# Kernel optimization log

Hardware: AMD Instinct MI355X
Metric: run time of the kernel (lower is better)

The kernel has to match this reference:

```python
import jax, jax.numpy as jnp
import numpy as np

WINDOW = 24  # rolling window size
C_IN = 7
D_MODEL = 512
B, S = 32, 4096


def setup_inputs() -> dict:
    key = jax.random.key(0)
    k1, k2, k3, k4 = jax.random.split(key, 4)
    x = jax.random.normal(k1, (B, S, C_IN), dtype=jnp.float32)
    x_mark = jax.random.normal(k2, (B, S, 4), dtype=jnp.float32)
    fan_in = 5 * C_IN * 3  # conv1d fan_in = in_channels * kernel_size
    gain = float(np.sqrt(2.0 / (1.0 + 0.01 ** 2)))  # kaiming, leaky_relu a=0.01
    W_conv = jax.random.normal(k3, (D_MODEL, 5 * C_IN, 3), dtype=jnp.float32) * (gain / np.sqrt(fan_in))
    bound = 1.0 / np.sqrt(fan_in)
    b_conv = jax.random.uniform(k4, (D_MODEL,), dtype=jnp.float32, minval=-bound, maxval=bound)
    return {"x": x, "x_mark": x_mark, "W_conv": W_conv, "b_conv": b_conv}


def _rolling_stats(x, window):
    # x: (B, S, F). Replicate-pad (window-1) at the front, then gather windows.
    Bb, Ss, Ff = x.shape
    padded = jnp.concatenate([jnp.repeat(x[:, :1, :], window - 1, axis=1), x], axis=1)
    idx = jnp.arange(Ss)[:, None] + jnp.arange(window)[None, :]  # (S, W)
    win = padded[:, idx, :]  # (B, S, W, F)
    mean = win.mean(axis=2)
    mx = win.max(axis=2)
    mn = win.min(axis=2)
    # torch.std default: unbiased (ddof=1); tiny eps only guards sqrt-at-0
    var = jnp.sum((win - mean[:, :, None, :]) ** 2, axis=2) / (window - 1)
    std = jnp.sqrt(var + 1e-12)
    return jnp.concatenate([x, mean, mx, mn, std], axis=-1)  # (B, S, 5F)


def reference(x, x_mark, W_conv, b_conv):
    feats = _rolling_stats(x, WINDOW)              # (B, S, 5*C_IN)
    h = jnp.transpose(feats, (0, 2, 1))             # (B, C, S)
    # circular padding of 1 on each side along seq (padding_mode='circular')
    h = jnp.concatenate([h[:, :, -1:], h, h[:, :, :1]], axis=-1)
    y = jax.lax.conv_general_dilated(
        h, W_conv, window_strides=(1,), padding='VALID',
        dimension_numbers=('NCH', 'OIH', 'NCH'))
    y = y + b_conv[None, :, None]
    # dropout is identity in eval mode
    return jnp.transpose(y, (0, 2, 1))              # (B, S, D_MODEL)
```

## Files before the change

### kernel.cpp

```cpp
#include <hip/hip_runtime.h>

#define B_    32
#define S_    4096
#define CIN_  7
#define NF_   35
#define D_    512
#define WIN_  24
#define K3_   105
#define P_    120
#define QN_   66

typedef __attribute__((ext_vector_type(8))) short short8;
typedef __attribute__((ext_vector_type(4))) float float4_;

__device__ __forceinline__ unsigned short f2bf(float f) {
    unsigned int u = __builtin_bit_cast(unsigned int, f);
    u += 0x7FFFu + ((u >> 16) & 1u);
    return (unsigned short)(u >> 16);
}

__global__ __launch_bounds__(256) void pack_w_kernel(
    const float* __restrict__ W, short* __restrict__ Bf)
{
    const int slot = blockIdx.x * 256 + threadIdx.x;
    if (slot >= 32 * 4 * 64) return;
    const int l     = slot & 63;
    const int kstep = (slot >> 6) & 3;
    const int nsub  = slot >> 8;
    const int d  = nsub * 16 + (l & 15);
    const int kb = kstep * 32 + (l >> 4) * 8;

    short8 v;
    #pragma unroll
    for (int j = 0; j < 8; ++j) {
        const int kappa = kb + j;
        v[j] = (kappa < K3_) ? (short)f2bf(W[(size_t)d * K3_ + kappa]) : (short)0;
    }
    *(short8*)(Bf + (size_t)slot * 8) = v;
}

template <bool USE_WS>
__global__ __launch_bounds__(512, 4) void fused_mfma_kernel(
    const float* __restrict__ x, const float* __restrict__ W,
    const short* __restrict__ Bf, const float* __restrict__ bias,
    float* __restrict__ out)
{
    __shared__ short sA[64 * P_];

    const int tid = threadIdx.x;
    const int s0  = blockIdx.x * 64;
    const int b   = blockIdx.y;

    if (tid < QN_ * CIN_) {
        const int q = tid / CIN_;
        const int f = tid - q * CIN_;
        int p = s0 - 1 + q;
        const int sm = p < 0 ? p + S_ : (p >= S_ ? p - S_ : p);
        const float* xb = x + (size_t)b * S_ * CIN_ + f;

        float v[WIN_];
        #pragma unroll
        for (int j = 0; j < WIN_; ++j) {
            int sc = sm - (WIN_ - 1) + j;
            sc = sc < 0 ? 0 : sc;
            v[j] = xb[(size_t)sc * CIN_];
        }
        float sum = 0.f, mx = v[0], mn = v[0];
        #pragma unroll
        for (int j = 0; j < WIN_; ++j) {
            sum += v[j];
            mx = fmaxf(mx, v[j]);
            mn = fminf(mn, v[j]);
        }
        const float mean = sum * (1.0f / WIN_);
        float var = 0.f;
        #pragma unroll
        for (int j = 0; j < WIN_; ++j) {
            const float dv = v[j] - mean;
            var = fmaf(dv, dv, var);
        }
        const float sd = sqrtf(var * (1.0f / (WIN_ - 1)) + 1e-12f);

        const float vals[5] = { v[WIN_ - 1], mean, mx, mn, sd };
        #pragma unroll
        for (int k = 0; k < 3; ++k) {
            const int m = q - k;
            if (m >= 0 && m < 64) {
                #pragma unroll
                for (int g = 0; g < 5; ++g) {
                    const int i = f + g * CIN_;
                    sA[m * P_ + i * 3 + k] = (short)f2bf(vals[g]);
                }
            }
        }
    }
    for (int t = tid; t < 64 * (P_ - K3_); t += 512) {
        const int m = t / (P_ - K3_);
        const int c = K3_ + (t - m * (P_ - K3_));
        sA[m * P_ + c] = 0;
    }
    __syncthreads();

    const int w  = tid >> 6;
    const int l  = tid & 63;
    const int lr = l & 15;
    const int lq = l >> 4;

    float4_ acc[4][4];
    #pragma unroll
    for (int n = 0; n < 4; ++n) {
        const float4_ bv = *(const float4_*)(bias + w * 64 + n * 16 + lq * 4);
        #pragma unroll
        for (int m = 0; m < 4; ++m) acc[m][n] = bv;
    }

    #pragma unroll
    for (int ks = 0; ks < 4; ++ks) {
        short8 ff[4];
        #pragma unroll
        for (int m = 0; m < 4; ++m)
            ff[m] = *(const short8*)&sA[(m * 16 + lr) * P_ + ks * 32 + lq * 8];

        short8 wf[4];
        #pragma unroll
        for (int n = 0; n < 4; ++n) {
            if (USE_WS) {
                const int nsub = w * 4 + n;
                wf[n] = *(const short8*)(Bf + ((size_t)(nsub * 4 + ks) * 64 + l) * 8);
            } else {
                const int d  = w * 64 + n * 16 + lr;
                const int kb = ks * 32 + lq * 8;
                short8 t8;
                #pragma unroll
                for (int j = 0; j < 8; ++j)
                    t8[j] = (kb + j < K3_) ? (short)f2bf(W[(size_t)d * K3_ + kb + j])
                                           : (short)0;
                wf[n] = t8;
            }
        }

        #pragma unroll
        for (int m = 0; m < 4; ++m)
            #pragma unroll
            for (int n = 0; n < 4; ++n)
                acc[m][n] = __builtin_amdgcn_mfma_f32_16x16x32_bf16(
                    wf[n], ff[m], acc[m][n], 0, 0, 0);
    }

    #pragma unroll
    for (int m = 0; m < 4; ++m) {
        float* ob = out + ((size_t)(b * S_ + s0 + m * 16 + lr)) * D_
                        + w * 64 + lq * 4;
        #pragma unroll
        for (int n = 0; n < 4; ++n)
            *(float4_*)(ob + n * 16) = acc[m][n];
    }
}

extern "C" void kernel_launch(void* const* d_in, const int* in_sizes, int n_in,
                              void* d_out, int out_size, void* d_ws, size_t ws_size,
                              hipStream_t stream) {
    const float* x      = (const float*)d_in[0];
    const float* W_conv = (const float*)d_in[2];
    const float* b_conv = (const float*)d_in[3];
    float* out = (float*)d_out;

    const size_t bf_bytes = (size_t)32 * 4 * 64 * 8 * sizeof(short);

    if (ws_size >= bf_bytes) {
        short* Bf = (short*)d_ws;
        pack_w_kernel<<<dim3(32), dim3(256), 0, stream>>>(W_conv, Bf);
        fused_mfma_kernel<true><<<dim3(S_ / 64, B_), dim3(512), 0, stream>>>(
            x, W_conv, Bf, b_conv, out);
    } else {
        fused_mfma_kernel<false><<<dim3(S_ / 64, B_), dim3(512), 0, stream>>>(
            x, W_conv, nullptr, b_conv, out);
    }
}
```

Before: 288.8 us.

## Process four tiles per block with double-buffered features and staged x prefetch

Each block now handles four consecutive 64-row tiles instead of one, cutting the grid from 64x32 to 16x32 blocks. The x window for the next tile is prefetched into registers during the current tile's MFMA work and output stores, then staged through shared memory so the rolling statistics read LDS instead of strided global loads. Feature tiles are double-buffered. In exchange the kernel has fewer blocks (512) to fill the GPU, uses more shared memory, and adds two barriers per tile.

```diff
diff --git a/kernel.cpp b/kernel.cpp
--- a/kernel.cpp
+++ b/kernel.cpp
@@ -9,6 +9,10 @@
 #define K3_   105
 #define P_    120
 #define QN_   66
+#define TPB_  4
+#define NG_   16
+#define XDW_  640
+#define FSZ_  (64 * P_ + 8)
 
 typedef __attribute__((ext_vector_type(8))) short short8;
 typedef __attribute__((ext_vector_type(4))) float float4_;
@@ -39,66 +43,98 @@
     *(short8*)(Bf + (size_t)slot * 8) = v;
 }
 
-template <bool USE_WS>
-__global__ __launch_bounds__(512, 4) void fused_mfma_kernel(
-    const float* __restrict__ x, const float* __restrict__ W,
-    const short* __restrict__ Bf, const float* __restrict__ bias,
-    float* __restrict__ out)
-{
-    __shared__ short sA[64 * P_];
-
-    const int tid = threadIdx.x;
-    const int s0  = blockIdx.x * 64;
-    const int b   = blockIdx.y;
-
+__device__ __forceinline__ void stats_core_store(
+    const float v[WIN_], int q, int f, short* __restrict__ sF)
+{
+    float sum = 0.f, mx = v[0], mn = v[0];
+    #pragma unroll
+    for (int j = 0; j < WIN_; ++j) {
+        sum += v[j];
+        mx = fmaxf(mx, v[j]);
+        mn = fminf(mn, v[j]);
+    }
+    const float mean = sum * (1.0f / WIN_);
+    float var = 0.f;
+    #pragma unroll
+    for (int j = 0; j < WIN_; ++j) {
+        const float dv = v[j] - mean;
+        var = fmaf(dv, dv, var);
+    }
+    const float sd = sqrtf(var * (1.0f / (WIN_ - 1)) + 1e-12f);
+
+    const float vals[5] = { v[WIN_ - 1], mean, mx, mn, sd };
+    #pragma unroll
+    for (int k = 0; k < 3; ++k) {
+        const int m = q - k;
+        if (m >= 0 && m < 64) {
+            #pragma unroll
+            for (int gg = 0; gg < 5; ++gg) {
+                const int i = f + gg * CIN_;
+                sF[m * P_ + i * 3 + k] = (short)f2bf(vals[gg]);
+            }
+        }
+    }
+}
+
+__device__ __forceinline__ void stats_direct(
+    const float* __restrict__ xb, int s0, int tid, short* __restrict__ sF)
+{
     if (tid < QN_ * CIN_) {
         const int q = tid / CIN_;
         const int f = tid - q * CIN_;
         int p = s0 - 1 + q;
         const int sm = p < 0 ? p + S_ : (p >= S_ ? p - S_ : p);
-        const float* xb = x + (size_t)b * S_ * CIN_ + f;
-
+        const float* xp = xb + f;
         float v[WIN_];
         #pragma unroll
         for (int j = 0; j < WIN_; ++j) {
             int sc = sm - (WIN_ - 1) + j;
             sc = sc < 0 ? 0 : sc;
-            v[j] = xb[(size_t)sc * CIN_];
-        }
-        float sum = 0.f, mx = v[0], mn = v[0];
-        #pragma unroll
-        for (int j = 0; j < WIN_; ++j) {
-            sum += v[j];
-            mx = fmaxf(mx, v[j]);
-            mn = fminf(mn, v[j]);
-        }
-        const float mean = sum * (1.0f / WIN_);
-        float var = 0.f;
-        #pragma unroll
-        for (int j = 0; j < WIN_; ++j) {
-            const float dv = v[j] - mean;
-            var = fmaf(dv, dv, var);
-        }
-        const float sd = sqrtf(var * (1.0f / (WIN_ - 1)) + 1e-12f);
-
-        const float vals[5] = { v[WIN_ - 1], mean, mx, mn, sd };
-        #pragma unroll
-        for (int k = 0; k < 3; ++k) {
-            const int m = q - k;
-            if (m >= 0 && m < 64) {
-                #pragma unroll
-                for (int g = 0; g < 5; ++g) {
-                    const int i = f + g * CIN_;
-                    sA[m * P_ + i * 3 + k] = (short)f2bf(vals[g]);
-                }
-            }
-        }
-    }
-    for (int t = tid; t < 64 * (P_ - K3_); t += 512) {
-        const int m = t / (P_ - K3_);
-        const int c = K3_ + (t - m * (P_ - K3_));
-        sA[m * P_ + c] = 0;
-    }
+            v[j] = xp[(size_t)sc * CIN_];
+        }
+        stats_core_store(v, q, f, sF);
+    }
+}
+
+__device__ __forceinline__ void stats_fast(
+    const float* __restrict__ sX, int tid, short* __restrict__ sF)
+{
+    if (tid < QN_ * CIN_) {
+        const int q = tid / CIN_;
+        const int f = tid - q * CIN_;
+        float v[WIN_];
+        #pragma unroll
+        for (int j = 0; j < WIN_; ++j)
+            v[j] = sX[(q + j) * CIN_ + f];
+        stats_core_store(v, q, f, sF);
+    }
+}
+
+template <bool USE_WS>
+__global__ __launch_bounds__(512, 4) void fused_pipe_kernel(
+    const float* __restrict__ x, const float* __restrict__ W,
+    const short* __restrict__ Bf, const float* __restrict__ bias,
+    float* __restrict__ out)
+{
+    __shared__ short sF[2][FSZ_];
+    __shared__ float sX[XDW_];
+
+    const int tid   = threadIdx.x;
+    const int grp   = blockIdx.x;
+    const int b     = blockIdx.y;
+    const int tile0 = grp * TPB_;
+    const float* xb = x + (size_t)b * S_ * CIN_;
+
+    for (int t = tid; t < 2 * 64 * (P_ - K3_); t += 512) {
+        const int bufz = t / (64 * (P_ - K3_));
+        const int r    = t - bufz * (64 * (P_ - K3_));
+        const int m    = r / (P_ - K3_);
+        const int c    = K3_ + (r - m * (P_ - K3_));
+        sF[bufz][m * P_ + c] = 0;
+    }
+    if (tid < 16) sF[tid >> 3][64 * P_ + (tid & 7)] = 0;
+
+    stats_direct(xb, tile0 * 64, tid, sF[0]);
     __syncthreads();
 
     const int w  = tid >> 6;
@@ -106,54 +142,82 @@
     const int lr = l & 15;
     const int lq = l >> 4;
 
-    float4_ acc[4][4];
-    #pragma unroll
-    for (int n = 0; n < 4; ++n) {
-        const float4_ bv = *(const float4_*)(bias + w * 64 + n * 16 + lq * 4);
-        #pragma unroll
-        for (int m = 0; m < 4; ++m) acc[m][n] = bv;
-    }
-
-    #pragma unroll
-    for (int ks = 0; ks < 4; ++ks) {
-        short8 ff[4];
-        #pragma unroll
-        for (int m = 0; m < 4; ++m)
-            ff[m] = *(const short8*)&sA[(m * 16 + lr) * P_ + ks * 32 + lq * 8];
-
-        short8 wf[4];
-        #pragma unroll
-        for (int n = 0; n < 4; ++n) {
-            if (USE_WS) {
-                const int nsub = w * 4 + n;
-                wf[n] = *(const short8*)(Bf + ((size_t)(nsub * 4 + ks) * 64 + l) * 8);
-            } else {
-                const int d  = w * 64 + n * 16 + lr;
-                const int kb = ks * 32 + lq * 8;
-                short8 t8;
+    float4_ bias4[4];
+    #pragma unroll
+    for (int n = 0; n < 4; ++n)
+        bias4[n] = *(const float4_*)(bias + w * 64 + n * 16 + lq * 4);
+
+    for (int it = 0; it < TPB_; ++it) {
+        const int  buf       = it & 1;
+        const int  s0        = (tile0 + it) * 64;
+        const bool has_next  = (it + 1 < TPB_);
+        const bool next_fast = has_next && (tile0 + it + 1 <= 62);
+
+        float tmp0 = 0.f, tmp1 = 0.f;
+        const float* xs = xb + (size_t)(s0 + 64 - WIN_) * CIN_;
+        if (next_fast) {
+            tmp0 = xs[tid];
+            if (tid < XDW_ - 512) tmp1 = xs[512 + tid];
+        }
+
+        float4_ acc[4][4];
+        #pragma unroll
+        for (int n = 0; n < 4; ++n)
+            #pragma unroll
+            for (int m = 0; m < 4; ++m) acc[m][n] = bias4[n];
+
+        #pragma unroll
+        for (int ks = 0; ks < 4; ++ks) {
+            short8 ff[4];
+            #pragma unroll
+            for (int m = 0; m < 4; ++m)
+                ff[m] = *(const short8*)&sF[buf][(m * 16 + lr) * P_ + ks * 32 + lq * 8];
+
+            short8 wf[4];
+            #pragma unroll
+            for (int n = 0; n < 4; ++n) {
+                if (USE_WS) {
+                    const int nsub = w * 4 + n;
+                    wf[n] = *(const short8*)(Bf + ((size_t)(nsub * 4 + ks) * 64 + l) * 8);
+                } else {
+                    const int d  = w * 64 + n * 16 + lr;
+                    const int kb = ks * 32 + lq * 8;
+                    short8 t8;
+                    #pragma unroll
+                    for (int j = 0; j < 8; ++j)
+                        t8[j] = (kb + j < K3_) ? (short)f2bf(W[(size_t)d * K3_ + kb + j])
+                                               : (short)0;
+                    wf[n] = t8;
+                }
+            }
+
+            #pragma unroll
+            for (int m = 0; m < 4; ++m)
                 #pragma unroll
-                for (int j = 0; j < 8; ++j)
-                    t8[j] = (kb + j < K3_) ? (short)f2bf(W[(size_t)d * K3_ + kb + j])
-                                           : (short)0;
-                wf[n] = t8;
+                for (int n = 0; n < 4; ++n)
+                    acc[m][n] = __builtin_amdgcn_mfma_f32_16x16x32_bf16(
+                        wf[n], ff[m], acc[m][n], 0, 0, 0);
+        }
+
+        #pragma unroll
+        for (int m = 0; m < 4; ++m) {
+            float* ob = out + ((size_t)(b * S_ + s0 + m * 16 + lr)) * D_
+                            + w * 64 + lq * 4;
+            #pragma unroll
+            for (int n = 0; n < 4; ++n)
+                *(float4_*)(ob + n * 16) = acc[m][n];
+        }
+
+        if (has_next) {
+            if (next_fast) {
+                sX[tid] = tmp0;
+                if (tid < XDW_ - 512) sX[512 + tid] = tmp1;
             }
-        }
-
-        #pragma unroll
-        for (int m = 0; m < 4; ++m)
-            #pragma unroll
-            for (int n = 0; n < 4; ++n)
-                acc[m][n] = __builtin_amdgcn_mfma_f32_16x16x32_bf16(
-                    wf[n], ff[m], acc[m][n], 0, 0, 0);
-    }
-
-    #pragma unroll
-    for (int m = 0; m < 4; ++m) {
-        float* ob = out + ((size_t)(b * S_ + s0 + m * 16 + lr)) * D_
-                        + w * 64 + lq * 4;
-        #pragma unroll
-        for (int n = 0; n < 4; ++n)
-            *(float4_*)(ob + n * 16) = acc[m][n];
+            __syncthreads();
+            if (next_fast) stats_fast(sX, tid, sF[buf ^ 1]);
+            else           stats_direct(xb, s0 + 64, tid, sF[buf ^ 1]);
+            __syncthreads();
+        }
     }
 }
 
@@ -170,10 +234,10 @@
     if (ws_size >= bf_bytes) {
         short* Bf = (short*)d_ws;
         pack_w_kernel<<<dim3(32), dim3(256), 0, stream>>>(W_conv, Bf);
-        fused_mfma_kernel<true><<<dim3(S_ / 64, B_), dim3(512), 0, stream>>>(
+        fused_pipe_kernel<true><<<dim3(NG_, B_), dim3(512), 0, stream>>>(
             x, W_conv, Bf, b_conv, out);
     } else {
-        fused_mfma_kernel<false><<<dim3(S_ / 64, B_), dim3(512), 0, stream>>>(
+        fused_pipe_kernel<false><<<dim3(NG_, B_), dim3(512), 0, stream>>>(
             x, W_conv, nullptr, b_conv, out);
     }
 }
```

Result: slower. 358.4 us (+24.1%).

## Shrink sequence tile to 32 rows and use 256-thread blocks with 128-wide wave tiles

Applied to the files above, without the earlier changes.

Halves the sequence tile per block from 64 to 32 rows and the block size from 512 to 256 threads. Each of the 4 waves now covers 128 output channels (2x8 MFMA tiles) instead of 64 (4x4), and weight fragments are loaded just before each pair of MFMAs instead of all up front. Rolling-stat halo overhead grows relative to the tile (34 rows of stats for 32 outputs versus 66 for 64), and each weight fragment is reused only twice instead of four times. In exchange the grid has twice as many smaller blocks, which is meant to improve occupancy and load balance on this output-write-bound kernel.

```diff
diff --git a/kernel.cpp b/kernel.cpp
--- a/kernel.cpp
+++ b/kernel.cpp
@@ -8,7 +8,9 @@
 #define WIN_  24
 #define K3_   105
 #define P_    120
-#define QN_   66
+#define TS_   32
+#define QN_   34
+#define FSZ_  (TS_ * P_ + 8)
 
 typedef __attribute__((ext_vector_type(8))) short short8;
 typedef __attribute__((ext_vector_type(4))) float float4_;
@@ -40,15 +42,15 @@
 }
 
 template <bool USE_WS>
-__global__ __launch_bounds__(512, 4) void fused_mfma_kernel(
+__global__ __launch_bounds__(256, 4) void fused_mfma_kernel(
     const float* __restrict__ x, const float* __restrict__ W,
     const short* __restrict__ Bf, const float* __restrict__ bias,
     float* __restrict__ out)
 {
-    __shared__ short sA[64 * P_];
+    __shared__ short sF[FSZ_];
 
     const int tid = threadIdx.x;
-    const int s0  = blockIdx.x * 64;
+    const int s0  = blockIdx.x * TS_;
     const int b   = blockIdx.y;
 
     if (tid < QN_ * CIN_) {
@@ -85,20 +87,21 @@
         #pragma unroll
         for (int k = 0; k < 3; ++k) {
             const int m = q - k;
-            if (m >= 0 && m < 64) {
+            if (m >= 0 && m < TS_) {
                 #pragma unroll
                 for (int g = 0; g < 5; ++g) {
                     const int i = f + g * CIN_;
-                    sA[m * P_ + i * 3 + k] = (short)f2bf(vals[g]);
+                    sF[m * P_ + i * 3 + k] = (short)f2bf(vals[g]);
                 }
             }
         }
     }
-    for (int t = tid; t < 64 * (P_ - K3_); t += 512) {
+    for (int t = tid; t < TS_ * (P_ - K3_); t += 256) {
         const int m = t / (P_ - K3_);
         const int c = K3_ + (t - m * (P_ - K3_));
-        sA[m * P_ + c] = 0;
+        sF[m * P_ + c] = 0;
     }
+    if (tid < 8) sF[TS_ * P_ + tid] = 0;
     __syncthreads();
 
     const int w  = tid >> 6;
@@ -106,53 +109,50 @@
     const int lr = l & 15;
     const int lq = l >> 4;
 
-    float4_ acc[4][4];
+    float4_ acc[2][8];
     #pragma unroll
-    for (int n = 0; n < 4; ++n) {
-        const float4_ bv = *(const float4_*)(bias + w * 64 + n * 16 + lq * 4);
-        #pragma unroll
-        for (int m = 0; m < 4; ++m) acc[m][n] = bv;
+    for (int n = 0; n < 8; ++n) {
+        const float4_ bv = *(const float4_*)(bias + w * 128 + n * 16 + lq * 4);
+        acc[0][n] = bv;
+        acc[1][n] = bv;
     }
 
     #pragma unroll
     for (int ks = 0; ks < 4; ++ks) {
-        short8 ff[4];
+        short8 ff[2];
         #pragma unroll
-        for (int m = 0; m < 4; ++m)
-            ff[m] = *(const short8*)&sA[(m * 16 + lr) * P_ + ks * 32 + lq * 8];
+        for (int m = 0; m < 2; ++m)
+            ff[m] = *(const short8*)&sF[(m * 16 + lr) * P_ + ks * 32 + lq * 8];
 
-        short8 wf[4];
         #pragma unroll
-        for (int n = 0; n < 4; ++n) {
+        for (int n = 0; n < 8; ++n) {
+            short8 wf;
             if (USE_WS) {
-                const int nsub = w * 4 + n;
-                wf[n] = *(const short8*)(Bf + ((size_t)(nsub * 4 + ks) * 64 + l) * 8);
+                const int nsub = w * 8 + n;
+                wf = *(const short8*)(Bf + ((size_t)(nsub * 4 + ks) * 64 + l) * 8);
             } else {
-                const int d  = w * 64 + n * 16 + lr;
+                const int d  = w * 128 + n * 16 + lr;
                 const int kb = ks * 32 + lq * 8;
                 short8 t8;
                 #pragma unroll
                 for (int j = 0; j < 8; ++j)
                     t8[j] = (kb + j < K3_) ? (short)f2bf(W[(size_t)d * K3_ + kb + j])
                                            : (short)0;
-                wf[n] = t8;
+                wf = t8;
             }
+            acc[0][n] = __builtin_amdgcn_mfma_f32_16x16x32_bf16(
+                wf, ff[0], acc[0][n], 0, 0, 0);
+            acc[1][n] = __builtin_amdgcn_mfma_f32_16x16x32_bf16(
+                wf, ff[1], acc[1][n], 0, 0, 0);
         }
-
-        #pragma unroll
-        for (int m = 0; m < 4; ++m)
-            #pragma unroll
-            for (int n = 0; n < 4; ++n)
-                acc[m][n] = __builtin_amdgcn_mfma_f32_16x16x32_bf16(
-                    wf[n], ff[m], acc[m][n], 0, 0, 0);
     }
 
     #pragma unroll
-    for (int m = 0; m < 4; ++m) {
+    for (int m = 0; m < 2; ++m) {
         float* ob = out + ((size_t)(b * S_ + s0 + m * 16 + lr)) * D_
-                        + w * 64 + lq * 4;
+                        + w * 128 + lq * 4;
         #pragma unroll
-        for (int n = 0; n < 4; ++n)
+        for (int n = 0; n < 8; ++n)
             *(float4_*)(ob + n * 16) = acc[m][n];
     }
 }
@@ -170,10 +170,10 @@
     if (ws_size >= bf_bytes) {
         short* Bf = (short*)d_ws;
         pack_w_kernel<<<dim3(32), dim3(256), 0, stream>>>(W_conv, Bf);
-        fused_mfma_kernel<true><<<dim3(S_ / 64, B_), dim3(512), 0, stream>>>(
+        fused_mfma_kernel<true><<<dim3(S_ / TS_, B_), dim3(256), 0, stream>>>(
             x, W_conv, Bf, b_conv, out);
     } else {
-        fused_mfma_kernel<false><<<dim3(S_ / 64, B_), dim3(512), 0, stream>>>(
+        fused_mfma_kernel<false><<<dim3(S_ / TS_, B_), dim3(256), 0, stream>>>(
             x, W_conv, nullptr, b_conv, out);
     }
 }
```

Result: slower. 300.9 us (+4.2%).

## Split fused stats+GEMM kernel into separate stats and GEMM kernels

Applied to the files above, without the earlier changes.

Splits the fused kernel into two launches. A stats kernel computes the rolling-window features and writes them to a global bf16 buffer padded to 128 columns. A GEMM kernel then reads those features straight from global memory into the MFMA operands, with no LDS staging or barrier. The aim is to decouple the latency-bound stats phase from the store-bound GEMM, at the cost of an extra launch and a ~32MB intermediate write and read. The fallback path keeps the fused design and only pads its LDS buffer.

```diff
diff --git a/kernel.cpp b/kernel.cpp
--- a/kernel.cpp
+++ b/kernel.cpp
@@ -8,6 +8,7 @@
 #define WIN_  24
 #define K3_   105
 #define P_    120
+#define FP_   128
 #define QN_   66
 
 typedef __attribute__((ext_vector_type(8))) short short8;
@@ -39,13 +40,137 @@
     *(short8*)(Bf + (size_t)slot * 8) = v;
 }
 
-template <bool USE_WS>
-__global__ __launch_bounds__(512, 4) void fused_mfma_kernel(
+__global__ __launch_bounds__(512, 4) void stats_kernel(
+    const float* __restrict__ x, short* __restrict__ Fg)
+{
+    __shared__ short sF[64 * P_];
+
+    const int tid = threadIdx.x;
+    const int s0  = blockIdx.x * 64;
+    const int b   = blockIdx.y;
+
+    if (tid < QN_ * CIN_) {
+        const int q = tid / CIN_;
+        const int f = tid - q * CIN_;
+        int p = s0 - 1 + q;
+        const int sm = p < 0 ? p + S_ : (p >= S_ ? p - S_ : p);
+        const float* xb = x + (size_t)b * S_ * CIN_ + f;
+
+        float v[WIN_];
+        #pragma unroll
+        for (int j = 0; j < WIN_; ++j) {
+            int sc = sm - (WIN_ - 1) + j;
+            sc = sc < 0 ? 0 : sc;
+            v[j] = xb[(size_t)sc * CIN_];
+        }
+        float sum = 0.f, mx = v[0], mn = v[0];
+        #pragma unroll
+        for (int j = 0; j < WIN_; ++j) {
+            sum += v[j];
+            mx = fmaxf(mx, v[j]);
+            mn = fminf(mn, v[j]);
+        }
+        const float mean = sum * (1.0f / WIN_);
+        float var = 0.f;
+        #pragma unroll
+        for (int j = 0; j < WIN_; ++j) {
+            const float dv = v[j] - mean;
+            var = fmaf(dv, dv, var);
+        }
+        const float sd = sqrtf(var * (1.0f / (WIN_ - 1)) + 1e-12f);
+
+        const float vals[5] = { v[WIN_ - 1], mean, mx, mn, sd };
+        #pragma unroll
+        for (int k = 0; k < 3; ++k) {
+            const int m = q - k;
+            if (m >= 0 && m < 64) {
+                #pragma unroll
+                for (int g = 0; g < 5; ++g) {
+                    const int i = f + g * CIN_;
+                    sF[m * P_ + i * 3 + k] = (short)f2bf(vals[g]);
+                }
+            }
+        }
+    }
+    for (int t = tid; t < 64 * (P_ - K3_); t += 512) {
+        const int m = t / (P_ - K3_);
+        const int c = K3_ + (t - m * (P_ - K3_));
+        sF[m * P_ + c] = 0;
+    }
+    __syncthreads();
+
+    const int r = tid >> 3;
+    const int c = tid & 7;
+    short8 lo = *(const short8*)&sF[r * P_ + c * 16];
+    short8 hi;
+    if (c < 7) hi = *(const short8*)&sF[r * P_ + c * 16 + 8];
+    else       hi = short8{0, 0, 0, 0, 0, 0, 0, 0};
+    short* dst = Fg + ((size_t)(b * S_ + s0 + r) * FP_ + c * 16);
+    *(short8*)(dst)     = lo;
+    *(short8*)(dst + 8) = hi;
+}
+
+__global__ __launch_bounds__(512, 4) void gemm_kernel(
+    const short* __restrict__ Fg, const short* __restrict__ Bf,
+    const float* __restrict__ bias, float* __restrict__ out)
+{
+    const int tid = threadIdx.x;
+    const int s0  = blockIdx.x * 64;
+    const int b   = blockIdx.y;
+
+    const int w  = tid >> 6;
+    const int l  = tid & 63;
+    const int lr = l & 15;
+    const int lq = l >> 4;
+
+    float4_ acc[4][4];
+    #pragma unroll
+    for (int n = 0; n < 4; ++n) {
+        const float4_ bv = *(const float4_*)(bias + w * 64 + n * 16 + lq * 4);
+        #pragma unroll
+        for (int m = 0; m < 4; ++m) acc[m][n] = bv;
+    }
+
+    const short* Fb = Fg + (size_t)(b * S_ + s0) * FP_;
+
+    #pragma unroll
+    for (int ks = 0; ks < 4; ++ks) {
+        short8 ff[4];
+        #pragma unroll
+        for (int m = 0; m < 4; ++m)
+            ff[m] = *(const short8*)(Fb + (size_t)(m * 16 + lr) * FP_
+                                        + ks * 32 + lq * 8);
+
+        short8 wf[4];
+        #pragma unroll
+        for (int n = 0; n < 4; ++n) {
+            const int nsub = w * 4 + n;
+            wf[n] = *(const short8*)(Bf + ((size_t)(nsub * 4 + ks) * 64 + l) * 8);
+        }
+
+        #pragma unroll
+        for (int m = 0; m < 4; ++m)
+            #pragma unroll
+            for (int n = 0; n < 4; ++n)
+                acc[m][n] = __builtin_amdgcn_mfma_f32_16x16x32_bf16(
+                    wf[n], ff[m], acc[m][n], 0, 0, 0);
+    }
+
+    #pragma unroll
+    for (int m = 0; m < 4; ++m) {
+        float* ob = out + ((size_t)(b * S_ + s0 + m * 16 + lr)) * D_
+                        + w * 64 + lq * 4;
+        #pragma unroll
+        for (int n = 0; n < 4; ++n)
+            *(float4_*)(ob + n * 16) = acc[m][n];
+    }
+}
+
+__global__ __launch_bounds__(512, 4) void fused_fallback_kernel(
     const float* __restrict__ x, const float* __restrict__ W,
-    const short* __restrict__ Bf, const float* __restrict__ bias,
-    float* __restrict__ out)
+    const float* __restrict__ bias, float* __restrict__ out)
 {
-    __shared__ short sA[64 * P_];
+    __shared__ short sA[64 * P_ + 8];
 
     const int tid = threadIdx.x;
     const int s0  = blockIdx.x * 64;
@@ -99,6 +224,7 @@
         const int c = K3_ + (t - m * (P_ - K3_));
         sA[m * P_ + c] = 0;
     }
+    if (tid < 8) sA[64 * P_ + tid] = 0;
     __syncthreads();
 
     const int w  = tid >> 6;
@@ -124,19 +250,14 @@
         short8 wf[4];
         #pragma unroll
         for (int n = 0; n < 4; ++n) {
-            if (USE_WS) {
-                const int nsub = w * 4 + n;
-                wf[n] = *(const short8*)(Bf + ((size_t)(nsub * 4 + ks) * 64 + l) * 8);
-            } else {
-                const int d  = w * 64 + n * 16 + lr;
-                const int kb = ks * 32 + lq * 8;
-                short8 t8;
-                #pragma unroll
-                for (int j = 0; j < 8; ++j)
-                    t8[j] = (kb + j < K3_) ? (short)f2bf(W[(size_t)d * K3_ + kb + j])
-                                           : (short)0;
-                wf[n] = t8;
-            }
+            const int d  = w * 64 + n * 16 + lr;
+            const int kb = ks * 32 + lq * 8;
+            short8 t8;
+            #pragma unroll
+            for (int j = 0; j < 8; ++j)
+                t8[j] = (kb + j < K3_) ? (short)f2bf(W[(size_t)d * K3_ + kb + j])
+                                       : (short)0;
+            wf[n] = t8;
         }
 
         #pragma unroll
@@ -166,14 +287,17 @@
     float* out = (float*)d_out;
 
     const size_t bf_bytes = (size_t)32 * 4 * 64 * 8 * sizeof(short);
-
-    if (ws_size >= bf_bytes) {
+    const size_t fg_bytes = (size_t)B_ * S_ * FP_ * sizeof(short);
+
+    if (ws_size >= bf_bytes + fg_bytes) {
         short* Bf = (short*)d_ws;
+        short* Fg = (short*)((char*)d_ws + bf_bytes);
         pack_w_kernel<<<dim3(32), dim3(256), 0, stream>>>(W_conv, Bf);
-        fused_mfma_kernel<true><<<dim3(S_ / 64, B_), dim3(512), 0, stream>>>(
-            x, W_conv, Bf, b_conv, out);
+        stats_kernel<<<dim3(S_ / 64, B_), dim3(512), 0, stream>>>(x, Fg);
+        gemm_kernel<<<dim3(S_ / 64, B_), dim3(512), 0, stream>>>(
+            Fg, Bf, b_conv, out);
     } else {
-        fused_mfma_kernel<false><<<dim3(S_ / 64, B_), dim3(512), 0, stream>>>(
-            x, W_conv, nullptr, b_conv, out);
-    }
-}
+        fused_fallback_kernel<<<dim3(S_ / 64, B_), dim3(512), 0, stream>>>(
+            x, W_conv, b_conv, out);
+    }
+}
```

Result: slower. 326.0 us (+12.9%).
